# Kernel optimization log

Measured on AMD Instinct MI355X. Metric: run time of the kernel, lower is better.

The kernel has to match this reference:

```python
import jax, jax.numpy as jnp
import numpy as np

EPS = 1e-5
N_NODES = 100000
C_IN = 128
C_OUT = 128
N_EDGES = 3200000


def setup_inputs() -> dict:
    key = jax.random.key(0)
    k1, k2, k3 = jax.random.split(key, 3)
    x = jax.random.normal(k1, (N_NODES, C_IN), dtype=jnp.float32)
    edge_index = jax.random.randint(k2, (2, N_EDGES), 0, N_NODES, dtype=jnp.int64)
    # BatchNorm1d affine params
    gamma = jnp.ones((C_IN,), dtype=jnp.float32)
    beta = jnp.zeros((C_IN,), dtype=jnp.float32)
    # GCNConv linear weight (glorot) and bias
    limit = np.sqrt(6.0 / (C_IN + C_OUT)).astype(np.float32)
    W = jax.random.uniform(k3, (C_IN, C_OUT), minval=-limit, maxval=limit, dtype=jnp.float32)
    b = jnp.zeros((C_OUT,), dtype=jnp.float32)
    return {"x": x, "edge_index": edge_index, "gamma": gamma, "beta": beta, "W": W, "b": b}


def reference(x, edge_index, gamma, beta, W, b):
    n = x.shape[0]
    # --- BatchNorm1d (training mode: batch statistics, biased variance) ---
    mean = jnp.mean(x, axis=0)
    var = jnp.mean(jnp.square(x - mean), axis=0)
    xn = (x - mean) * jax.lax.rsqrt(var + EPS) * gamma + beta
    # --- GCNConv: linear, add self-loops, symmetric normalization, scatter-add ---
    h = xn @ W  # [n, C_out]
    loops = jnp.arange(n, dtype=edge_index.dtype)
    row = jnp.concatenate([edge_index[0], loops])  # source nodes
    col = jnp.concatenate([edge_index[1], loops])  # target nodes
    deg = jax.ops.segment_sum(jnp.ones_like(col, dtype=h.dtype), col, num_segments=n)
    dis = jnp.where(deg > 0, jax.lax.rsqrt(jnp.maximum(deg, 1.0)), 0.0)
    norm = dis[row] * dis[col]  # [E+n]
    msg = h[row] * norm[:, None]  # gather + scale
    out = jax.ops.segment_sum(msg, col, num_segments=n) + b  # scatter-add
    return jax.nn.relu(out)
```

## Files before the change

kernel.cpp:

```cpp
#include <hip/hip_runtime.h>

#define EPS_BN 1e-5f
#define C 128
#define CG 32
#define CAP 6144
#define NBLK 256

typedef __attribute__((ext_vector_type(8))) short bf16x8;
typedef __attribute__((ext_vector_type(4))) float f32x4;

__device__ inline unsigned bf16_rne(float f) {
  unsigned u = __float_as_uint(f);
  return (u + 0x7FFFu + ((u >> 16) & 1u)) >> 16;
}
__device__ inline float bf16_f(unsigned h) { return __uint_as_float(h << 16); }

__global__ void k_init(float* __restrict__ sums) {
  int i = blockIdx.x * blockDim.x + threadIdx.x;
  if (i < 256) sums[i] = 0.0f;
}

__global__ void k_stats(const float4* __restrict__ x4, float* __restrict__ sums, int n) {
  __shared__ float4 s_s[256];
  __shared__ float4 s_q[256];
  int t = threadIdx.x;
  int cg = t & 31;
  int rl = t >> 5;
  float4 s = make_float4(0.f, 0.f, 0.f, 0.f);
  float4 q = make_float4(0.f, 0.f, 0.f, 0.f);
  for (int r = blockIdx.x * 8 + rl; r < n; r += gridDim.x * 8) {
    float4 v = x4[(size_t)r * CG + cg];
    s.x += v.x; s.y += v.y; s.z += v.z; s.w += v.w;
    q.x += v.x * v.x; q.y += v.y * v.y; q.z += v.z * v.z; q.w += v.w * v.w;
  }
  s_s[t] = s; s_q[t] = q;
  __syncthreads();
  if (t < 32) {
    for (int j = 1; j < 8; ++j) {
      float4 a = s_s[t + 32 * j];
      float4 b = s_q[t + 32 * j];
      s.x += a.x; s.y += a.y; s.z += a.z; s.w += a.w;
      q.x += b.x; q.y += b.y; q.z += b.z; q.w += b.w;
    }
    atomicAdd(&sums[t * 4 + 0], s.x);
    atomicAdd(&sums[t * 4 + 1], s.y);
    atomicAdd(&sums[t * 4 + 2], s.z);
    atomicAdd(&sums[t * 4 + 3], s.w);
    atomicAdd(&sums[C + t * 4 + 0], q.x);
    atomicAdd(&sums[C + t * 4 + 1], q.y);
    atomicAdd(&sums[C + t * 4 + 2], q.z);
    atomicAdd(&sums[C + t * 4 + 3], q.w);
  }
}

__global__ void k_finalize(const float* __restrict__ sums,
                           const float* __restrict__ gamma,
                           const float* __restrict__ beta,
                           float* __restrict__ scale, float* __restrict__ shift,
                           int n) {
  int c = threadIdx.x;
  if (c < C) {
    float inv_n = 1.0f / (float)n;
    float mean = sums[c] * inv_n;
    float var = sums[C + c] * inv_n - mean * mean;
    float rstd = rsqrtf(var + EPS_BN);
    float sc = gamma[c] * rstd;
    scale[c] = sc;
    shift[c] = beta[c] - mean * sc;
  }
}

__global__ void k_hist(const int* __restrict__ col, int* __restrict__ histG,
                       int E, int NB, int chunk) {
  __shared__ int h[800];
  int b = blockIdx.x, t = threadIdx.x;
  for (int i = t; i < NB; i += 256) h[i] = 0;
  __syncthreads();
  int s = b * chunk, eend = min(E, s + chunk);
  for (int e = s + t; e < eend; e += 256) atomicAdd(&h[col[e] >> 7], 1);
  __syncthreads();
  for (int i = t; i < NB; i += 256) histG[b * NB + i] = h[i];
}

__global__ void k_scanH(int* __restrict__ histG, int* __restrict__ btot, int NB) {
  __shared__ int sh[NBLK];
  int q = blockIdx.x, t = threadIdx.x;
  int v = histG[t * NB + q];
  sh[t] = v;
  __syncthreads();
  for (int off = 1; off < NBLK; off <<= 1) {
    int a = (t >= off) ? sh[t - off] : 0;
    __syncthreads();
    sh[t] += a;
    __syncthreads();
  }
  histG[t * NB + q] = sh[t] - v;
  if (t == NBLK - 1) btot[q] = sh[t];
}

__global__ void k_scanB(const int* __restrict__ btot, int* __restrict__ boffs,
                        int NB, int E) {
  __shared__ int sh[1024];
  int t = threadIdx.x;
  int v = (t < NB) ? btot[t] : 0;
  sh[t] = v;
  __syncthreads();
  for (int off = 1; off < 1024; off <<= 1) {
    int a = (t >= off) ? sh[t - off] : 0;
    __syncthreads();
    sh[t] += a;
    __syncthreads();
  }
  if (t < NB) boffs[t] = sh[t] - v;
  if (t == 0) boffs[NB] = E;
}

__global__ void k_part(const int* __restrict__ row, const int* __restrict__ col,
                       const int* __restrict__ histG, const int* __restrict__ boffs,
                       unsigned* __restrict__ binned, int E, int NB, int chunk) {
  __shared__ int cur[800];
  int b = blockIdx.x, t = threadIdx.x;
  for (int i = t; i < NB; i += 256) cur[i] = boffs[i] + histG[b * NB + i];
  __syncthreads();
  int s = b * chunk, eend = min(E, s + chunk);
  for (int e = s + t; e < eend; e += 256) {
    int c = col[e];
    int pos = atomicAdd(&cur[c >> 7], 1);
    binned[pos] = ((unsigned)(c & 127) << 17) | (unsigned)row[e];
  }
}

__global__ __launch_bounds__(256) void k_reorder(
    unsigned* __restrict__ binned, const int* __restrict__ boffs,
    int* __restrict__ noffs, float* __restrict__ dis, int n, int E) {
  __shared__ int cnt[128];
  __shared__ int offs[128];
  __shared__ int cur[128];
  __shared__ int scn[128];
  __shared__ unsigned list[CAP];
  int b = blockIdx.x, t = threadIdx.x;
  if (t < 128) cnt[t] = 0;
  __syncthreads();
  int s = boffs[b], e = boffs[b + 1];
  for (int i = s + t; i < e; i += 256) atomicAdd(&cnt[binned[i] >> 17], 1);
  __syncthreads();
  if (t < 128) scn[t] = cnt[t];
  __syncthreads();
  for (int off = 1; off < 128; off <<= 1) {
    int a = (t >= off && t < 128) ? scn[t - off] : 0;
    __syncthreads();
    if (t < 128) scn[t] += a;
    __syncthreads();
  }
  if (t < 128) {
    offs[t] = scn[t] - cnt[t];
    cur[t] = scn[t] - cnt[t];
  }
  __syncthreads();
  for (int i = s + t; i < e; i += 256) {
    unsigned v = binned[i];
    int pos = atomicAdd(&cur[v >> 17], 1);
    if (pos < CAP) list[pos] = v & 0x1FFFFu;
  }
  __syncthreads();
  int len = e - s;
  for (int i = t; i < len; i += 256) binned[s + i] = list[i];
  int node = b * 128 + t;
  if (t < 128 && node < n) {
    noffs[node] = s + offs[t];
    dis[node] = rsqrtf((float)(cnt[t] + 1));
  }
  if (b == 0 && t == 0) noffs[n] = E;
}

__global__ void k_prep(const float2* __restrict__ x2, const float* __restrict__ dis,
                       const float2* __restrict__ scale2,
                       const float2* __restrict__ shift2,
                       unsigned* __restrict__ y, int n) {
  int idx = blockIdx.x * blockDim.x + threadIdx.x;
  int r = idx >> 6;
  if (r >= n) return;
  int lane = idx & 63;
  float d = dis[r];
  float2 v = x2[(size_t)r * 64 + lane];
  float2 sc = scale2[lane], sh = shift2[lane];
  float y0 = (v.x * sc.x + sh.x) * d;
  float y1 = (v.y * sc.y + sh.y) * d;
  y[(size_t)r * 64 + lane] = (bf16_rne(y1) << 16) | bf16_rne(y0);
}

__global__ __launch_bounds__(256) void k_G2(
    const unsigned* __restrict__ y, const unsigned* __restrict__ lst,
    const int* __restrict__ noffs, const float* __restrict__ dis,
    unsigned* __restrict__ ghi, unsigned* __restrict__ glo, int n) {
  int w = (blockIdx.x * blockDim.x + threadIdx.x) >> 6;
  if (w >= n) return;
  int lane = threadIdx.x & 63;
  int s = noffs[w], t = noffs[w + 1];
  float2 a0 = make_float2(0.f, 0.f), a1 = make_float2(0.f, 0.f);
  float2 a2 = make_float2(0.f, 0.f), a3 = make_float2(0.f, 0.f);
  int i = s;
  for (; i + 3 < t; i += 4) {
    int r0 = lst[i], r1 = lst[i + 1], r2 = lst[i + 2], r3 = lst[i + 3];
    unsigned u0 = y[(size_t)r0 * 64 + lane];
    unsigned u1 = y[(size_t)r1 * 64 + lane];
    unsigned u2 = y[(size_t)r2 * 64 + lane];
    unsigned u3 = y[(size_t)r3 * 64 + lane];
    a0.x += __uint_as_float(u0 << 16); a0.y += __uint_as_float(u0 & 0xFFFF0000u);
    a1.x += __uint_as_float(u1 << 16); a1.y += __uint_as_float(u1 & 0xFFFF0000u);
    a2.x += __uint_as_float(u2 << 16); a2.y += __uint_as_float(u2 & 0xFFFF0000u);
    a3.x += __uint_as_float(u3 << 16); a3.y += __uint_as_float(u3 & 0xFFFF0000u);
  }
  for (; i < t; ++i) {
    unsigned u = y[(size_t)lst[i] * 64 + lane];
    a0.x += __uint_as_float(u << 16); a0.y += __uint_as_float(u & 0xFFFF0000u);
  }
  unsigned uw = y[(size_t)w * 64 + lane];
  a0.x += __uint_as_float(uw << 16); a0.y += __uint_as_float(uw & 0xFFFF0000u);
  float dc = dis[w];
  float gx = dc * (a0.x + a1.x + a2.x + a3.x);
  float gy = dc * (a0.y + a1.y + a2.y + a3.y);
  unsigned hx = bf16_rne(gx), hy = bf16_rne(gy);
  unsigned lx = bf16_rne(gx - bf16_f(hx)), ly = bf16_rne(gy - bf16_f(hy));
  size_t o = (size_t)w * 64 + lane;
  ghi[o] = (hy << 16) | hx;
  glo[o] = (ly << 16) | lx;
}

__global__ __launch_bounds__(256) void k_gemmM(
    const unsigned* __restrict__ ghi, const unsigned* __restrict__ glo,
    const float* __restrict__ W, const float* __restrict__ bias,
    float* __restrict__ out, int n) {
  __shared__ __align__(16) unsigned short sGh[64][136];
  __shared__ __align__(16) unsigned short sGl[64][136];
  __shared__ __align__(16) unsigned short sWt[128][136];
  int t = threadIdx.x;
  int rowBase = blockIdx.x * 64;
  for (int i = t; i < 16384; i += 256) {
    int k = i >> 7, c = i & 127;
    sWt[c][k] = (unsigned short)bf16_rne(W[i]);
  }
  for (int i = t; i < 4096; i += 256) {
    int r = i >> 6, c = i & 63;
    int rw = rowBase + r;
    unsigned uh = 0, ul = 0;
    if (rw < n) {
      uh = ghi[(size_t)rw * 64 + c];
      ul = glo[(size_t)rw * 64 + c];
    }
    *(unsigned*)&sGh[r][c * 2] = uh;
    *(unsigned*)&sGl[r][c * 2] = ul;
  }
  __syncthreads();
  int w = t >> 6, l = t & 63;
  int m16 = l & 15, kb = l >> 4;
  int rtile = w * 16;
  f32x4 acc[8];
#pragma unroll
  for (int i = 0; i < 8; ++i) acc[i] = (f32x4){0.f, 0.f, 0.f, 0.f};
#pragma unroll
  for (int kt = 0; kt < 4; ++kt) {
    int koff = kt * 32 + kb * 8;
    bf16x8 ah = *(const bf16x8*)&sGh[rtile + m16][koff];
    bf16x8 al = *(const bf16x8*)&sGl[rtile + m16][koff];
#pragma unroll
    for (int nt = 0; nt < 8; ++nt) {
      bf16x8 bb = *(const bf16x8*)&sWt[nt * 16 + m16][koff];
      acc[nt] = __builtin_amdgcn_mfma_f32_16x16x32_bf16(ah, bb, acc[nt], 0, 0, 0);
      acc[nt] = __builtin_amdgcn_mfma_f32_16x16x32_bf16(al, bb, acc[nt], 0, 0, 0);
    }
  }
#pragma unroll
  for (int nt = 0; nt < 8; ++nt) {
    int colc = nt * 16 + m16;
    float bv = bias[colc];
#pragma unroll
    for (int reg = 0; reg < 4; ++reg) {
      int row = rowBase + rtile + kb * 4 + reg;
      if (row < n) {
        float o = acc[nt][reg] + bv;
        out[(size_t)row * C + colc] = fmaxf(o, 0.f);
      }
    }
  }
}

__global__ __launch_bounds__(256) void k_G(
    const unsigned* __restrict__ y, const unsigned* __restrict__ lst,
    const int* __restrict__ noffs, const float* __restrict__ dis,
    const float2* __restrict__ x2, const float2* __restrict__ scale2,
    const float2* __restrict__ shift2, float2* __restrict__ out2,
    int n, int useY) {
  int w = (blockIdx.x * blockDim.x + threadIdx.x) >> 6;
  if (w >= n) return;
  int lane = threadIdx.x & 63;
  int s = noffs[w], t = noffs[w + 1];
  float2 a0 = make_float2(0.f, 0.f), a1 = make_float2(0.f, 0.f);
  float2 a2 = make_float2(0.f, 0.f), a3 = make_float2(0.f, 0.f);
  if (useY) {
    int i = s;
    for (; i + 3 < t; i += 4) {
      int r0 = lst[i], r1 = lst[i + 1], r2 = lst[i + 2], r3 = lst[i + 3];
      unsigned u0 = y[(size_t)r0 * 64 + lane];
      unsigned u1 = y[(size_t)r1 * 64 + lane];
      unsigned u2 = y[(size_t)r2 * 64 + lane];
      unsigned u3 = y[(size_t)r3 * 64 + lane];
      a0.x += __uint_as_float(u0 << 16); a0.y += __uint_as_float(u0 & 0xFFFF0000u);
      a1.x += __uint_as_float(u1 << 16); a1.y += __uint_as_float(u1 & 0xFFFF0000u);
      a2.x += __uint_as_float(u2 << 16); a2.y += __uint_as_float(u2 & 0xFFFF0000u);
      a3.x += __uint_as_float(u3 << 16); a3.y += __uint_as_float(u3 & 0xFFFF0000u);
    }
    for (; i < t; ++i) {
      unsigned u = y[(size_t)lst[i] * 64 + lane];
      a0.x += __uint_as_float(u << 16); a0.y += __uint_as_float(u & 0xFFFF0000u);
    }
    float dc = dis[w];
    float2 o;
    o.x = dc * (a0.x + a1.x + a2.x + a3.x);
    o.y = dc * (a0.y + a1.y + a2.y + a3.y);
    out2[(size_t)w * 64 + lane] = o;
  } else {
    float sd = 0.f;
    for (int i = s; i < t; ++i) {
      int r = lst[i];
      float d = dis[r];
      float2 v = x2[(size_t)r * 64 + lane];
      a0.x += v.x * d; a0.y += v.y * d; sd += d;
    }
    float dc = dis[w];
    float2 sc = scale2[lane], sh = shift2[lane];
    float2 o;
    o.x = dc * (a0.x * sc.x + sd * sh.x);
    o.y = dc * (a0.y * sc.y + sd * sh.y);
    out2[(size_t)w * 64 + lane] = o;
  }
}

__global__ __launch_bounds__(256) void k_gemm(float* __restrict__ out,
                        const float4* __restrict__ x4,
                        const float* __restrict__ W,
                        const float* __restrict__ bias,
                        const float* __restrict__ scale,
                        const float* __restrict__ shift,
                        const float* __restrict__ dis, int n) {
  __shared__ float sW[64 * C];
  __shared__ float sG[32 * C];
  int t = threadIdx.x;
  int rowBase = blockIdx.x * 32;

  const float4* scale4 = (const float4*)scale;
  const float4* shift4 = (const float4*)shift;
  float4* sG4 = (float4*)sG;
  float4* sW4 = (float4*)sW;
  const float4* W4 = (const float4*)W;
  const float4* out4 = (const float4*)out;

  for (int i = t; i < 32 * CG; i += 256) {
    int r = i >> 5, g = i & 31;
    int rw = rowBase + r;
    float4 acc = make_float4(0.f, 0.f, 0.f, 0.f);
    if (rw < n) {
      acc = out4[(size_t)rw * CG + g];
      float4 xv = x4[(size_t)rw * CG + g];
      float d = dis[rw];
      float inv = d * d;
      float4 sc = scale4[g];
      float4 sh = shift4[g];
      acc.x += (xv.x * sc.x + sh.x) * inv;
      acc.y += (xv.y * sc.y + sh.y) * inv;
      acc.z += (xv.z * sc.z + sh.z) * inv;
      acc.w += (xv.w * sc.w + sh.w) * inv;
    }
    sG4[i] = acc;
  }

  int tx = t & 127;
  int ty = t >> 7;
  float acc[16];
#pragma unroll
  for (int i = 0; i < 16; ++i) acc[i] = 0.f;

  for (int kc = 0; kc < 2; ++kc) {
    for (int i = t; i < 64 * C / 4; i += 256) sW4[i] = W4[kc * 2048 + i];
    __syncthreads();
#pragma unroll 4
    for (int k = 0; k < 64; ++k) {
      float w = sW[k * C + tx];
#pragma unroll
      for (int rr = 0; rr < 16; ++rr)
        acc[rr] += sG[(rr * 2 + ty) * C + kc * 64 + k] * w;
    }
    __syncthreads();
  }

  float bv = bias[tx];
#pragma unroll
  for (int rr = 0; rr < 16; ++rr) {
    int rw = rowBase + rr * 2 + ty;
    if (rw < n) {
      float o = acc[rr] + bv;
      out[(size_t)rw * C + tx] = o > 0.f ? o : 0.f;
    }
  }
}

extern "C" void kernel_launch(void* const* d_in, const int* in_sizes, int n_in,
                              void* d_out, int out_size, void* d_ws, size_t ws_size,
                              hipStream_t stream) {
  const float* x = (const float*)d_in[0];
  const int* edge = (const int*)d_in[1];
  const float* gamma = (const float*)d_in[2];
  const float* beta = (const float*)d_in[3];
  const float* W = (const float*)d_in[4];
  const float* bias = (const float*)d_in[5];
  float* out = (float*)d_out;

  int n = in_sizes[0] / C;
  int E = in_sizes[1] / 2;
  int NB = (n + 127) / 128;
  int chunk = (E + NBLK - 1) / NBLK;

  float* ws = (float*)d_ws;
  float* sums = ws;
  float* scale = ws + 256;
  float* shift = ws + 384;
  float* dis = ws + 512;
  int* btot = (int*)(ws + 512 + n);
  int* boffs = btot + NB;
  int* noffs = boffs + NB + 1;
  int* histG = noffs + n + 1;
  unsigned* binned = (unsigned*)(histG + (size_t)NBLK * NB);
  unsigned* y = binned + E;
  unsigned* ghi = y + (size_t)n * 64;
  unsigned* glo = ghi + (size_t)n * 64;

  size_t base = (size_t)512 + n + NB + (NB + 1) + (n + 1) +
                (size_t)NBLK * NB + E;
  size_t need_old = base + (size_t)n * 64;
  size_t need_new = base + (size_t)n * 64 * 3;
  int mode = (ws_size >= need_new * 4) ? 2 : (ws_size >= need_old * 4) ? 1 : 0;

  k_init<<<1, 256, 0, stream>>>(sums);
  k_stats<<<256, 256, 0, stream>>>((const float4*)x, sums, n);
  k_finalize<<<1, 128, 0, stream>>>(sums, gamma, beta, scale, shift, n);
  k_hist<<<NBLK, 256, 0, stream>>>(edge + E, histG, E, NB, chunk);
  k_scanH<<<NB, NBLK, 0, stream>>>(histG, btot, NB);
  k_scanB<<<1, 1024, 0, stream>>>(btot, boffs, NB, E);
  k_part<<<NBLK, 256, 0, stream>>>(edge, edge + E, histG, boffs, binned, E, NB, chunk);
  k_reorder<<<NB, 256, 0, stream>>>(binned, boffs, noffs, dis, n, E);
  if (mode >= 1) {
    k_prep<<<(n * 64 + 255) / 256, 256, 0, stream>>>(
        (const float2*)x, dis, (const float2*)scale, (const float2*)shift, y, n);
  }
  if (mode == 2) {
    k_G2<<<(n * 64 + 255) / 256, 256, 0, stream>>>(y, binned, noffs, dis,
                                                   ghi, glo, n);
    k_gemmM<<<(n + 63) / 64, 256, 0, stream>>>(ghi, glo, W, bias, out, n);
  } else {
    k_G<<<(n * 64 + 255) / 256, 256, 0, stream>>>(
        y, binned, noffs, dis, (const float2*)x, (const float2*)scale,
        (const float2*)shift, (float2*)out, n, mode);
    k_gemm<<<(n + 31) / 32, 256, 0, stream>>>(out, (const float4*)x, W, bias,
                                              scale, shift, dis, n);
  }
}
```

Before: 349.0 us.

## Sort each destination bin's edges by source-row chunk to improve gather locality

The per-bin reorder kernel now counting-sorts edges by (source chunk, destination node) using 16 source-row chunks of 8192 nodes, and writes per-chunk offsets into a new noffs2 table. The gather kernel walks each node's neighbours chunk by chunk. Blocks processed at the same time therefore touch similar regions of the bf16 feature array, which is meant to raise L2 hit rates for the random gathers. In exchange there are larger shared-memory histograms, a 256-wide scan, a bigger offsets table, and extra loop and tail overhead per node in the gather.

```diff
diff --git a/kernel.cpp b/kernel.cpp
--- a/kernel.cpp
+++ b/kernel.cpp
@@ -5,6 +5,7 @@
 #define CG 32
 #define CAP 6144
 #define NBLK 256
+#define CHK 16
 
 typedef __attribute__((ext_vector_type(8))) short bf16x8;
 typedef __attribute__((ext_vector_type(4))) float f32x4;
@@ -130,7 +131,68 @@
   }
 }
 
-__global__ __launch_bounds__(256) void k_reorder(
+__global__ __launch_bounds__(256) void k_reorderC(
+    unsigned* __restrict__ binned, const int* __restrict__ boffs,
+    int* __restrict__ noffs2, float* __restrict__ dis, int n, int E, int NB) {
+  __shared__ int cnt[2048];
+  __shared__ int cur[2048];
+  __shared__ int tsum[256];
+  __shared__ int deg[128];
+  __shared__ unsigned list[CAP];
+  int b = blockIdx.x, t = threadIdx.x;
+  for (int i = t; i < 2048; i += 256) cnt[i] = 0;
+  __syncthreads();
+  int s = boffs[b], e = boffs[b + 1];
+  for (int i = s + t; i < e; i += 256) {
+    unsigned v = binned[i];
+    int key = (int)((v & 0x1FFFFu) >> 13) * 128 + (int)(v >> 17);
+    atomicAdd(&cnt[key], 1);
+  }
+  __syncthreads();
+  if (t < 128) {
+    int d = 0;
+#pragma unroll
+    for (int c = 0; c < CHK; ++c) d += cnt[c * 128 + t];
+    deg[t] = d;
+  }
+  __syncthreads();
+  int b8 = t * 8;
+  int tot = 0;
+#pragma unroll
+  for (int j = 0; j < 8; ++j) tot += cnt[b8 + j];
+  tsum[t] = tot;
+  __syncthreads();
+  for (int off = 1; off < 256; off <<= 1) {
+    int a = (t >= off) ? tsum[t - off] : 0;
+    __syncthreads();
+    tsum[t] += a;
+    __syncthreads();
+  }
+  int run = tsum[t] - tot;
+#pragma unroll
+  for (int j = 0; j < 8; ++j) {
+    int c0 = cnt[b8 + j];
+    cnt[b8 + j] = run;
+    cur[b8 + j] = run;
+    run += c0;
+  }
+  __syncthreads();
+  for (int i = s + t; i < e; i += 256) {
+    unsigned v = binned[i];
+    int key = (int)((v & 0x1FFFFu) >> 13) * 128 + (int)(v >> 17);
+    int pos = atomicAdd(&cur[key], 1);
+    if (pos < CAP) list[pos] = v & 0x1FFFFu;
+  }
+  __syncthreads();
+  int len = e - s;
+  for (int i = t; i < len; i += 256) binned[s + i] = list[i];
+  for (int k = t; k < 2048; k += 256) noffs2[b * 2048 + k] = s + cnt[k];
+  int node = b * 128 + t;
+  if (t < 128 && node < n) dis[node] = rsqrtf((float)(deg[t] + 1));
+  if (b == NB - 1 && t == 0) noffs2[NB * 2048] = E;
+}
+
+__global__ __launch_bounds__(256) void k_reorderO(
     unsigned* __restrict__ binned, const int* __restrict__ boffs,
     int* __restrict__ noffs, float* __restrict__ dis, int n, int E) {
   __shared__ int cnt[128];
@@ -191,32 +253,47 @@
 
 __global__ __launch_bounds__(256) void k_G2(
     const unsigned* __restrict__ y, const unsigned* __restrict__ lst,
-    const int* __restrict__ noffs, const float* __restrict__ dis,
+    const int* __restrict__ noffs2, const float* __restrict__ dis,
     unsigned* __restrict__ ghi, unsigned* __restrict__ glo, int n) {
   int w = (blockIdx.x * blockDim.x + threadIdx.x) >> 6;
   if (w >= n) return;
   int lane = threadIdx.x & 63;
-  int s = noffs[w], t = noffs[w + 1];
+  int nb2 = (w >> 7) * 2048 + (w & 127);
   float2 a0 = make_float2(0.f, 0.f), a1 = make_float2(0.f, 0.f);
   float2 a2 = make_float2(0.f, 0.f), a3 = make_float2(0.f, 0.f);
-  int i = s;
-  for (; i + 3 < t; i += 4) {
-    int r0 = lst[i], r1 = lst[i + 1], r2 = lst[i + 2], r3 = lst[i + 3];
-    unsigned u0 = y[(size_t)r0 * 64 + lane];
-    unsigned u1 = y[(size_t)r1 * 64 + lane];
-    unsigned u2 = y[(size_t)r2 * 64 + lane];
-    unsigned u3 = y[(size_t)r3 * 64 + lane];
-    a0.x += __uint_as_float(u0 << 16); a0.y += __uint_as_float(u0 & 0xFFFF0000u);
-    a1.x += __uint_as_float(u1 << 16); a1.y += __uint_as_float(u1 & 0xFFFF0000u);
-    a2.x += __uint_as_float(u2 << 16); a2.y += __uint_as_float(u2 & 0xFFFF0000u);
-    a3.x += __uint_as_float(u3 << 16); a3.y += __uint_as_float(u3 & 0xFFFF0000u);
-  }
-  for (; i < t; ++i) {
-    unsigned u = y[(size_t)lst[i] * 64 + lane];
+#pragma unroll 1
+  for (int c = 0; c < CHK; ++c) {
+    int si = noffs2[nb2 + c * 128];
+    int ei = noffs2[nb2 + c * 128 + 1];
+    int i = si;
+    for (; i + 3 < ei; i += 4) {
+      int r0 = lst[i], r1 = lst[i + 1], r2 = lst[i + 2], r3 = lst[i + 3];
+      unsigned u0 = y[(size_t)r0 * 64 + lane];
+      unsigned u1 = y[(size_t)r1 * 64 + lane];
+      unsigned u2 = y[(size_t)r2 * 64 + lane];
+      unsigned u3 = y[(size_t)r3 * 64 + lane];
+      a0.x += __uint_as_float(u0 << 16); a0.y += __uint_as_float(u0 & 0xFFFF0000u);
+      a1.x += __uint_as_float(u1 << 16); a1.y += __uint_as_float(u1 & 0xFFFF0000u);
+      a2.x += __uint_as_float(u2 << 16); a2.y += __uint_as_float(u2 & 0xFFFF0000u);
+      a3.x += __uint_as_float(u3 << 16); a3.y += __uint_as_float(u3 & 0xFFFF0000u);
+    }
+    if (i + 1 < ei) {
+      int r0 = lst[i], r1 = lst[i + 1];
+      unsigned u0 = y[(size_t)r0 * 64 + lane];
+      unsigned u1 = y[(size_t)r1 * 64 + lane];
+      a0.x += __uint_as_float(u0 << 16); a0.y += __uint_as_float(u0 & 0xFFFF0000u);
+      a1.x += __uint_as_float(u1 << 16); a1.y += __uint_as_float(u1 & 0xFFFF0000u);
+      i += 2;
+    }
+    if (i < ei) {
+      unsigned u = y[(size_t)lst[i] * 64 + lane];
+      a0.x += __uint_as_float(u << 16); a0.y += __uint_as_float(u & 0xFFFF0000u);
+    }
+  }
+  {
+    unsigned u = y[(size_t)w * 64 + lane];
     a0.x += __uint_as_float(u << 16); a0.y += __uint_as_float(u & 0xFFFF0000u);
   }
-  unsigned uw = y[(size_t)w * 64 + lane];
-  a0.x += __uint_as_float(uw << 16); a0.y += __uint_as_float(uw & 0xFFFF0000u);
   float dc = dis[w];
   float gx = dc * (a0.x + a1.x + a2.x + a3.x);
   float gy = dc * (a0.y + a1.y + a2.y + a3.y);
@@ -433,11 +510,12 @@
   unsigned* y = binned + E;
   unsigned* ghi = y + (size_t)n * 64;
   unsigned* glo = ghi + (size_t)n * 64;
+  int* noffs2 = (int*)(glo + (size_t)n * 64);
 
   size_t base = (size_t)512 + n + NB + (NB + 1) + (n + 1) +
                 (size_t)NBLK * NB + E;
   size_t need_old = base + (size_t)n * 64;
-  size_t need_new = base + (size_t)n * 64 * 3;
+  size_t need_new = base + (size_t)n * 64 * 3 + (size_t)NB * 2048 + 1;
   int mode = (ws_size >= need_new * 4) ? 2 : (ws_size >= need_old * 4) ? 1 : 0;
 
   k_init<<<1, 256, 0, stream>>>(sums);
@@ -447,16 +525,19 @@
   k_scanH<<<NB, NBLK, 0, stream>>>(histG, btot, NB);
   k_scanB<<<1, 1024, 0, stream>>>(btot, boffs, NB, E);
   k_part<<<NBLK, 256, 0, stream>>>(edge, edge + E, histG, boffs, binned, E, NB, chunk);
-  k_reorder<<<NB, 256, 0, stream>>>(binned, boffs, noffs, dis, n, E);
-  if (mode >= 1) {
+  if (mode == 2) {
+    k_reorderC<<<NB, 256, 0, stream>>>(binned, boffs, noffs2, dis, n, E, NB);
     k_prep<<<(n * 64 + 255) / 256, 256, 0, stream>>>(
         (const float2*)x, dis, (const float2*)scale, (const float2*)shift, y, n);
-  }
-  if (mode == 2) {
-    k_G2<<<(n * 64 + 255) / 256, 256, 0, stream>>>(y, binned, noffs, dis,
+    k_G2<<<(n * 64 + 255) / 256, 256, 0, stream>>>(y, binned, noffs2, dis,
                                                    ghi, glo, n);
     k_gemmM<<<(n + 63) / 64, 256, 0, stream>>>(ghi, glo, W, bias, out, n);
   } else {
+    k_reorderO<<<NB, 256, 0, stream>>>(binned, boffs, noffs, dis, n, E);
+    if (mode >= 1) {
+      k_prep<<<(n * 64 + 255) / 256, 256, 0, stream>>>(
+          (const float2*)x, dis, (const float2*)scale, (const float2*)shift, y, n);
+    }
     k_G<<<(n * 64 + 255) / 256, 256, 0, stream>>>(
         y, binned, noffs, dis, (const float2*)x, (const float2*)scale,
         (const float2*)shift, (float2*)out, n, mode);
```

Measured after the change: 442.3 us. +26.7%, slower.
